# Kernel tuning notes

Hardware: AMD Instinct MI355X
Metric: run time of the kernel (lower is better)

## Reference

```python
import jax, jax.numpy as jnp
import numpy as np

B, IN, OUT = 131072, 256, 256
BITWIDTH = 7.0


def setup_inputs() -> dict:
    key = jax.random.key(0)
    k1, k2 = jax.random.split(key)
    # simulated int8 activations (integer-valued float32)
    act_in = jax.random.randint(k1, (B, IN), -127, 128).astype(jnp.float32)
    # UniformWeights: xavier_uniform then weight_quant to the int8 grid
    limit = float(np.sqrt(6.0 / (IN + OUT)))
    w = jax.random.uniform(k2, (OUT, IN), minval=-limit, maxval=limit, dtype=jnp.float32)
    w_range = jnp.max(jnp.abs(w))
    weight_exp = (jnp.ceil(jnp.log2(w_range)) - 7.0).astype(jnp.int32)
    weight = jnp.round(w / w_range * 127.0)  # int8-valued float32 [OUT, IN]
    return {"act_in": act_in, "exp_in": jnp.int32(0), "weight": weight, "weight_exp": weight_exp}


def _round_shift(x, shift):
    # RoundShift: floor-div by 2**shift, add floor(|remainder| / 2**(shift-1)), clip to int8
    two_s = jnp.exp2(shift)
    rt = jnp.floor(x / two_s)
    prob = jnp.abs(x - rt * two_s)
    dec = jnp.floor(prob / jnp.exp2(shift - 1.0))
    return jnp.clip(rt + dec, -127.0, 127.0)


def reference(act_in, exp_in, weight, weight_exp):
    # int8 GEMM simulated in fp32 (exact: |acc| < 2^24)
    temp = act_in @ weight.T  # [B, OUT] int32 accumulator values
    # RangeEstimate: full-tensor abs-max -> bitwidth
    r = jnp.max(jnp.abs(temp))
    bw = jnp.where(r > 0, jnp.ceil(jnp.log2(jnp.maximum(r, 1.0))), 0.0)
    shift = bw - BITWIDTH
    pos = shift > 0
    safe_shift = jnp.maximum(shift, 1.0)
    rounded = _round_shift(temp, safe_shift)
    act_out = jnp.where(pos, rounded, temp).astype(jnp.int8)
    exp_sum = jnp.asarray(exp_in, jnp.int32) + jnp.asarray(weight_exp, jnp.int32)
    exp_out = (exp_sum + jnp.where(pos, shift, 0.0).astype(jnp.int32)).astype(jnp.int16)
    return act_out, exp_out
```

## Files before the change

### kernel.cpp

```cpp
#include <hip/hip_runtime.h>
#include <stdint.h>


#define M_ROWS 131072
#define NK 256
#define BM 64
#define AKP 264

typedef __attribute__((ext_vector_type(8))) short bf16x8;
typedef __attribute__((ext_vector_type(4))) float f32x4;
typedef __attribute__((ext_vector_type(4))) float fv4;
typedef __attribute__((ext_vector_type(4))) int iv4;
typedef __attribute__((ext_vector_type(4))) unsigned int u32x4;
typedef __attribute__((ext_vector_type(4))) unsigned short us4;

__device__ __forceinline__ uint32_t pack_bf16(float a, float b) {
  return (__float_as_uint(a) >> 16) | (__float_as_uint(b) & 0xFFFF0000u);
}

__global__ void wconv(const float* __restrict__ w, unsigned short* __restrict__ wb) {
  const int i = blockIdx.x * 256 + threadIdx.x;
  const fv4 f = ((const fv4*)w)[i];
  us4 o;
  o.x = (unsigned short)(__float_as_uint(f.x) >> 16);
  o.y = (unsigned short)(__float_as_uint(f.y) >> 16);
  o.z = (unsigned short)(__float_as_uint(f.z) >> 16);
  o.w = (unsigned short)(__float_as_uint(f.w) >> 16);
  ((us4*)wb)[i] = o;
}

__global__ __launch_bounds__(256) void gemm_store_max(
    const float* __restrict__ act,
    const unsigned short* __restrict__ wgtb,
    int* __restrict__ temp,
    int* __restrict__ gmax)
{
  __shared__ __align__(16) short As[BM * AKP];
  __shared__ int smax;

  const int tid = threadIdx.x;
  if (tid == 0) smax = 0;

  const int bm   = blockIdx.x * BM;
  const int lane = tid & 63;
  const int wave = tid >> 6;
  const int lm   = lane & 15;
  const int lk   = lane >> 4;
  const int wn   = wave * 64;

  {
    const int arow = tid >> 5;
    const int aseg = tid & 31;
    const float* pbase = act + (size_t)(bm + arow) * NK + aseg * 8;
#pragma unroll
    for (int j = 0; j < 8; ++j) {
      const float* p = pbase + (size_t)(j * 8) * NK;
      const fv4 f0 = *(const fv4*)p;
      const fv4 f1 = *((const fv4*)p + 1);
      uint32_t pk[4];
      pk[0] = pack_bf16(f0.x, f0.y); pk[1] = pack_bf16(f0.z, f0.w);
      pk[2] = pack_bf16(f1.x, f1.y); pk[3] = pack_bf16(f1.z, f1.w);
      *(u32x4*)&As[(arow + j * 8) * AKP + aseg * 8] = *(const u32x4*)pk;
    }
  }
  __syncthreads();

  f32x4 acc[4][4] = {};

  const unsigned short* bbase = wgtb + (size_t)(wn + lm) * NK + lk * 8;
#pragma unroll
  for (int k8 = 0; k8 < 8; ++k8) {
    const int kk = k8 * 32;
    bf16x8 af[4];
    u32x4 bf[4];
#pragma unroll
    for (int ni = 0; ni < 4; ++ni)
      bf[ni] = *(const u32x4*)(bbase + (size_t)(ni * 16) * NK + kk);
#pragma unroll
    for (int mi = 0; mi < 4; ++mi)
      af[mi] = *(const bf16x8*)&As[(mi * 16 + lm) * AKP + kk + lk * 8];
#pragma unroll
    for (int mi = 0; mi < 4; ++mi)
#pragma unroll
      for (int ni = 0; ni < 4; ++ni)
        acc[mi][ni] = __builtin_amdgcn_mfma_f32_16x16x32_bf16(
            af[mi], *(const bf16x8*)&bf[ni], acc[mi][ni], 0, 0, 0);
  }

  int imax = 0;
#pragma unroll
  for (int mi = 0; mi < 4; ++mi)
#pragma unroll
    for (int ni = 0; ni < 4; ++ni)
#pragma unroll
      for (int r = 0; r < 4; ++r) {
        const int iv = (int)acc[mi][ni][r];
        const int m = bm + mi * 16 + lk * 4 + r;
        const int n = wn + ni * 16 + lm;
        temp[(size_t)m * NK + n] = iv;
        const int a = iv < 0 ? -iv : iv;
        imax = a > imax ? a : imax;
      }
#pragma unroll
  for (int off = 32; off; off >>= 1) {
    const int o = __shfl_xor(imax, off, 64);
    imax = o > imax ? o : imax;
  }
  if (lane == 0) atomicMax(&smax, imax);
  __syncthreads();
  if (tid == 0) atomicMax(gmax, smax);
}

__global__ __launch_bounds__(256) void quant_stream(
    const int* __restrict__ temp, int* __restrict__ out,
    const int* __restrict__ gmax,
    const int* __restrict__ exp_in, const int* __restrict__ wexp)
{
  const int r = *gmax;
  const int bw = (r <= 1) ? 0 : (32 - __clz(r - 1));
  const int shift = bw - 7;
  const bool pos = shift > 0;
  const int s = shift < 1 ? 1 : shift;

  const int total4 = (M_ROWS * NK) / 4;
  const iv4* pin = (const iv4*)temp;
  iv4* pout = (iv4*)out;
  const int idx = blockIdx.x * blockDim.x + threadIdx.x;
  const int stride = gridDim.x * blockDim.x;

  for (int i = idx; i < total4; i += stride) {
    const iv4 t = pin[i];
    iv4 o;
#pragma unroll
    for (int j = 0; j < 4; ++j) {
      const int ti = t[j];
      int q;
      if (pos) {
        const int rt = ti >> s;
        const int dec = (ti - (rt << s)) >> (s - 1);
        q = rt + dec;
        q = q > 127 ? 127 : (q < -127 ? -127 : q);
      } else {
        q = (int)(signed char)(ti & 0xFF);
      }
      o[j] = q;
    }
    __builtin_nontemporal_store(o, &pout[i]);
  }

  if (idx == 0) {
    const int e = exp_in[0] + wexp[0] + (pos ? shift : 0);
    out[(size_t)M_ROWS * NK] = (int)(short)e;
  }
}

extern "C" void kernel_launch(void* const* d_in, const int* in_sizes, int n_in,
                              void* d_out, int out_size, void* d_ws, size_t ws_size,
                              hipStream_t stream) {
  const float* act   = (const float*)d_in[0];
  const int* exp_in  = (const int*)d_in[1];
  const float* wgt   = (const float*)d_in[2];
  const int* wexp    = (const int*)d_in[3];

  int* gmax          = (int*)d_ws;
  unsigned short* wb = (unsigned short*)((char*)d_ws + 4096);
  int* temp          = (int*)((char*)d_ws + (1 << 20));

  (void)hipMemsetAsync(d_ws, 0, sizeof(int), stream);
  wconv<<<dim3(64), dim3(256), 0, stream>>>(wgt, wb);
  gemm_store_max<<<dim3(M_ROWS / BM), dim3(256), 0, stream>>>(act, wb, temp, gmax);
  quant_stream<<<dim3(4096), dim3(256), 0, stream>>>(temp, (int*)d_out, gmax,
                                                     exp_in, wexp);
}
```

Before: 304.5 us.

## Swap MFMA operands for vector temp stores, prefetch weights, restructure quant loads

The GEMM now passes the weight fragment as the first MFMA operand, so each lane holds four consecutive output columns and can write the int32 accumulator tile with 16-byte vector stores instead of scalar stores. Activation global loads are issued into registers before the weight loads and bf16 packing, and the weight fragments are double-buffered across k-steps so the next step's loads overlap the current MFMAs. The quantization kernel drops the grid-stride loop: each thread handles four consecutive int4 vectors with all loads issued up front, on a grid twice as large. Holding the prefetched values raises register pressure.

```diff
diff --git a/kernel.cpp b/kernel.cpp
--- a/kernel.cpp
+++ b/kernel.cpp
@@ -48,34 +48,47 @@
   const int lk   = lane >> 4;
   const int wn   = wave * 64;
 
-  {
-    const int arow = tid >> 5;
-    const int aseg = tid & 31;
-    const float* pbase = act + (size_t)(bm + arow) * NK + aseg * 8;
+  const int arow = tid >> 5;
+  const int aseg = tid & 31;
+  const float* pbase = act + (size_t)(bm + arow) * NK + aseg * 8;
+  fv4 fr[16];
 #pragma unroll
-    for (int j = 0; j < 8; ++j) {
-      const float* p = pbase + (size_t)(j * 8) * NK;
-      const fv4 f0 = *(const fv4*)p;
-      const fv4 f1 = *((const fv4*)p + 1);
-      uint32_t pk[4];
-      pk[0] = pack_bf16(f0.x, f0.y); pk[1] = pack_bf16(f0.z, f0.w);
-      pk[2] = pack_bf16(f1.x, f1.y); pk[3] = pack_bf16(f1.z, f1.w);
-      *(u32x4*)&As[(arow + j * 8) * AKP + aseg * 8] = *(const u32x4*)pk;
-    }
+  for (int j = 0; j < 8; ++j) {
+    const float* p = pbase + (size_t)(j * 8) * NK;
+    fr[2 * j]     = *(const fv4*)p;
+    fr[2 * j + 1] = *((const fv4*)p + 1);
+  }
+
+  const unsigned short* bbase = wgtb + (size_t)(wn + lm) * NK + lk * 8;
+  bf16x8 bcur[4];
+#pragma unroll
+  for (int ni = 0; ni < 4; ++ni)
+    bcur[ni] = *(const bf16x8*)(bbase + (size_t)(ni * 16) * NK);
+
+#pragma unroll
+  for (int j = 0; j < 8; ++j) {
+    uint32_t pk[4];
+    pk[0] = pack_bf16(fr[2 * j].x, fr[2 * j].y);
+    pk[1] = pack_bf16(fr[2 * j].z, fr[2 * j].w);
+    pk[2] = pack_bf16(fr[2 * j + 1].x, fr[2 * j + 1].y);
+    pk[3] = pack_bf16(fr[2 * j + 1].z, fr[2 * j + 1].w);
+    *(u32x4*)&As[(arow + j * 8) * AKP + aseg * 8] = *(const u32x4*)pk;
   }
   __syncthreads();
 
   f32x4 acc[4][4] = {};
 
-  const unsigned short* bbase = wgtb + (size_t)(wn + lm) * NK + lk * 8;
 #pragma unroll
   for (int k8 = 0; k8 < 8; ++k8) {
+    bf16x8 bnxt[4];
+    if (k8 < 7) {
+      const int kkn = (k8 + 1) * 32;
+#pragma unroll
+      for (int ni = 0; ni < 4; ++ni)
+        bnxt[ni] = *(const bf16x8*)(bbase + (size_t)(ni * 16) * NK + kkn);
+    }
     const int kk = k8 * 32;
     bf16x8 af[4];
-    u32x4 bf[4];
-#pragma unroll
-    for (int ni = 0; ni < 4; ++ni)
-      bf[ni] = *(const u32x4*)(bbase + (size_t)(ni * 16) * NK + kk);
 #pragma unroll
     for (int mi = 0; mi < 4; ++mi)
       af[mi] = *(const bf16x8*)&As[(mi * 16 + lm) * AKP + kk + lk * 8];
@@ -84,23 +97,30 @@
 #pragma unroll
       for (int ni = 0; ni < 4; ++ni)
         acc[mi][ni] = __builtin_amdgcn_mfma_f32_16x16x32_bf16(
-            af[mi], *(const bf16x8*)&bf[ni], acc[mi][ni], 0, 0, 0);
+            bcur[ni], af[mi], acc[mi][ni], 0, 0, 0);
+    if (k8 < 7) {
+#pragma unroll
+      for (int ni = 0; ni < 4; ++ni) bcur[ni] = bnxt[ni];
+    }
   }
 
   int imax = 0;
 #pragma unroll
-  for (int mi = 0; mi < 4; ++mi)
+  for (int mi = 0; mi < 4; ++mi) {
+    const size_t rowoff = (size_t)(bm + mi * 16 + lm) * NK;
 #pragma unroll
-    for (int ni = 0; ni < 4; ++ni)
+    for (int ni = 0; ni < 4; ++ni) {
+      iv4 qv;
 #pragma unroll
       for (int r = 0; r < 4; ++r) {
         const int iv = (int)acc[mi][ni][r];
-        const int m = bm + mi * 16 + lk * 4 + r;
-        const int n = wn + ni * 16 + lm;
-        temp[(size_t)m * NK + n] = iv;
+        qv[r] = iv;
         const int a = iv < 0 ? -iv : iv;
         imax = a > imax ? a : imax;
       }
+      *(iv4*)&temp[rowoff + wn + ni * 16 + lk * 4] = qv;
+    }
+  }
 #pragma unroll
   for (int off = 32; off; off >>= 1) {
     const int o = __shfl_xor(imax, off, 64);
@@ -122,18 +142,20 @@
   const bool pos = shift > 0;
   const int s = shift < 1 ? 1 : shift;
 
-  const int total4 = (M_ROWS * NK) / 4;
-  const iv4* pin = (const iv4*)temp;
-  iv4* pout = (iv4*)out;
-  const int idx = blockIdx.x * blockDim.x + threadIdx.x;
-  const int stride = gridDim.x * blockDim.x;
+  const size_t t = (size_t)blockIdx.x * 256 + threadIdx.x;
+  const iv4* pin = (const iv4*)temp + t * 4;
+  iv4* pout = (iv4*)out + t * 4;
 
-  for (int i = idx; i < total4; i += stride) {
-    const iv4 t = pin[i];
+  iv4 v[4];
+#pragma unroll
+  for (int j = 0; j < 4; ++j) v[j] = pin[j];
+
+#pragma unroll
+  for (int j = 0; j < 4; ++j) {
     iv4 o;
 #pragma unroll
-    for (int j = 0; j < 4; ++j) {
-      const int ti = t[j];
+    for (int e = 0; e < 4; ++e) {
+      const int ti = v[j][e];
       int q;
       if (pos) {
         const int rt = ti >> s;
@@ -143,12 +165,12 @@
       } else {
         q = (int)(signed char)(ti & 0xFF);
       }
-      o[j] = q;
+      o[e] = q;
     }
-    __builtin_nontemporal_store(o, &pout[i]);
+    __builtin_nontemporal_store(o, &pout[j]);
   }
 
-  if (idx == 0) {
+  if (t == 0) {
     const int e = exp_in[0] + wexp[0] + (pos ? shift : 0);
     out[(size_t)M_ROWS * NK] = (int)(short)e;
   }
@@ -169,6 +191,6 @@
   (void)hipMemsetAsync(d_ws, 0, sizeof(int), stream);
   wconv<<<dim3(64), dim3(256), 0, stream>>>(wgt, wb);
   gemm_store_max<<<dim3(M_ROWS / BM), dim3(256), 0, stream>>>(act, wb, temp, gmax);
-  quant_stream<<<dim3(4096), dim3(256), 0, stream>>>(temp, (int*)d_out, gmax,
+  quant_stream<<<dim3(8192), dim3(256), 0, stream>>>(temp, (int*)d_out, gmax,
                                                      exp_in, wexp);
 }
```

Result: slower. 428.5 us (+40.7%).
